# Kernel optimization log

Measured on AMD Instinct MI355X. Metric: run time of the kernel, lower is better.

Reference implementation:

```python
import jax, jax.numpy as jnp
import numpy as np

B, C, N = 2, 1024, 80
D = 3 * C + 2  # 3074 token dim
DFF = 2048     # torch TransformerEncoderLayer default dim_feedforward
HW = 224
REFINE = 3
EPS = 1e-5


def _layernorm(x, g, b):
    m = jnp.mean(x, axis=-1, keepdims=True)
    v = jnp.mean((x - m) ** 2, axis=-1, keepdims=True)
    return g * (x - m) / jnp.sqrt(v + EPS) + b


def _pos_encoding(seq_len, dim):
    pos = jnp.arange(seq_len, dtype=jnp.float32)[:, None]
    div = jnp.exp(jnp.arange(0, dim, 2, dtype=jnp.float32) * (-np.log(10000.0) / dim))
    pe = jnp.zeros((seq_len, dim), dtype=jnp.float32)
    pe = pe.at[:, 0::2].set(jnp.sin(pos * div)).at[:, 1::2].set(jnp.cos(pos * div))
    return pe


def _forward(pre_f, curr_f, first_f, ln_g, ln_b, ipw, ipb, opw, opb,
             n1g, n1b, l1w, l1b, l2w, l2b, n2g, n2b, ow, ob,
             prev_b, first_b):
    # --- vectorized find_best_shift: batched circular L1 correlation ---
    idx = (jnp.arange(N)[None, :] - jnp.arange(N)[:, None]) % N  # [shift, pos]
    rolled = first_b[:, idx]                                     # [B, N, N, 2]
    dist = jnp.abs(prev_b[:, None] - rolled).sum(axis=(-1, -2))  # [B, N]
    best = jnp.argmin(dist, axis=1)                              # first min, like torch loop
    roll_idx = (jnp.arange(N)[None, :] - best[:, None]) % N      # [B, N]
    first_b = jax.vmap(lambda fb, ri: fb[ri])(first_b, roll_idx)

    # --- bilinear upsample to 224x224 (F.interpolate, align_corners=False) ---
    up = lambda f: jax.image.resize(f, (f.shape[0], f.shape[1], HW, HW), method='bilinear')
    pre_up, curr_up, first_up = up(pre_f), up(curr_f), up(first_f)

    # --- vectorized get_bou_features: [B,N,C] gather ---
    gather = jax.vmap(lambda f, b: f[:, b[:, 0], b[:, 1]].T)
    pre_q = gather(pre_up, prev_b)      # [B, N, C]
    first_q = gather(first_up, first_b)  # [B, N, C]

    pe = _pos_encoding(N, D)
    curr = prev_b.astype(jnp.float32)
    scale = 1.0 / jnp.sqrt(jnp.float32(D))
    results = []
    for _ in range(REFINE):
        bf = gather(curr_up, curr.astype(jnp.int32))          # [B, N, C]
        tokens = jnp.concatenate([pre_q, bf, curr, first_q], axis=-1)  # [B, N, D]
        tokens = _layernorm(tokens, ln_g, ln_b)
        tokens = tokens + pe[None]
        # --- TransformerEncoderLayer (post-norm, nhead=1, relu, eval/no dropout) ---
        qkv = tokens @ ipw.T + ipb
        q, k, v = jnp.split(qkv, 3, axis=-1)
        attn = jax.nn.softmax(jnp.einsum('bqd,bkd->bqk', q, k) * scale, axis=-1)
        a = jnp.einsum('bqk,bkd->bqd', attn, v) @ opw.T + opb
        x = _layernorm(tokens + a, n1g, n1b)
        ff = jax.nn.relu(x @ l1w.T + l1b) @ l2w.T + l2b
        x = _layernorm(x + ff, n2g, n2b)
        out = x @ ow.T + ob                                   # [B, N, 1026]
        curr = jnp.clip(curr + out[..., C:], 0.0, 223.0)
        pre_q = pre_q + out[..., :C]
        results.append(curr)
    return jnp.stack(results)  # [REFINE, B, N, 2]


def setup_inputs() -> dict:
    key = jax.random.key(0)
    ks = jax.random.split(key, 12)
    f = lambda i, s: jax.random.normal(ks[i], s, dtype=jnp.float32)
    w = lambda i, s: 0.02 * jax.random.normal(ks[i], s, dtype=jnp.float32)
    return {
        'pre_img_features': f(0, (B, C, 14, 14)),
        'curr_img_features': f(1, (B, C, 14, 14)),
        'first_img_features': f(2, (B, C, 14, 14)),
        'previous_boundary': jax.random.randint(ks[3], (B, N, 2), 0, HW),
        'first_boundary': jax.random.randint(ks[4], (B, N, 2), 0, HW),
        'ln_g': jnp.ones((D,), jnp.float32), 'ln_b': jnp.zeros((D,), jnp.float32),
        'in_proj_w': w(5, (3 * D, D)), 'in_proj_b': jnp.zeros((3 * D,), jnp.float32),
        'out_proj_w': w(6, (D, D)), 'out_proj_b': jnp.zeros((D,), jnp.float32),
        'norm1_g': jnp.ones((D,), jnp.float32), 'norm1_b': jnp.zeros((D,), jnp.float32),
        'lin1_w': w(7, (DFF, D)), 'lin1_b': jnp.zeros((DFF,), jnp.float32),
        'lin2_w': w(8, (D, DFF)), 'lin2_b': jnp.zeros((D,), jnp.float32),
        'norm2_g': jnp.ones((D,), jnp.float32), 'norm2_b': jnp.zeros((D,), jnp.float32),
        'out_w': w(9, (C + 2, D)), 'out_b': jnp.zeros((C + 2,), jnp.float32),
    }


def reference(pre_img_features, curr_img_features, first_img_features,
              previous_boundary, first_boundary,
              ln_g, ln_b, in_proj_w, in_proj_b, out_proj_w, out_proj_b,
              norm1_g, norm1_b, lin1_w, lin1_b, lin2_w, lin2_b,
              norm2_g, norm2_b, out_w, out_b):
    return _forward(pre_img_features, curr_img_features, first_img_features,
                    ln_g, ln_b, in_proj_w, in_proj_b, out_proj_w, out_proj_b,
                    norm1_g, norm1_b, lin1_w, lin1_b, lin2_w, lin2_b,
                    norm2_g, norm2_b, out_w, out_b,
                    previous_boundary, first_boundary)
```

## Files before the change

### kernel.cpp

```cpp
#include <hip/hip_runtime.h>
#include <math.h>

#define B_    2
#define C_    1024
#define N_    80
#define D_    3074
#define DFF_  2048
#define OD_   1026
#define QKV_  9222
#define M_    160
#define EPS_  1e-5f
#define KPD_  3104
#define SPL_  4

typedef __attribute__((ext_vector_type(8))) short bf16x8;
typedef __attribute__((ext_vector_type(4))) float f32x4;

__device__ inline short f2bf(float f) {
    unsigned u = __float_as_uint(f);
    u += 0x7fffu + ((u >> 16) & 1u);
    return (short)(u >> 16);
}

__device__ inline float wave_sum(float v) {
#pragma unroll
    for (int off = 32; off > 0; off >>= 1) v += __shfl_down(v, off, 64);
    return v;
}

__device__ inline float wave_max(float v) {
#pragma unroll
    for (int off = 32; off > 0; off >>= 1) v = fmaxf(v, __shfl_down(v, off, 64));
    return v;
}

__device__ inline void block_reduce_2(float& s, float& s2, float* red) {
    int tid = threadIdx.x;
    int lane = tid & 63, wid = tid >> 6;
    s = wave_sum(s);
    s2 = wave_sum(s2);
    if (lane == 0) { red[wid] = s; red[4 + wid] = s2; }
    __syncthreads();
    if (tid == 0) {
        red[8] = red[0] + red[1] + red[2] + red[3];
        red[9] = red[4] + red[5] + red[6] + red[7];
    }
    __syncthreads();
    s = red[8]; s2 = red[9];
}

__device__ inline void bilin_setup(int p, int& i0, int& i1, float& t) {
    float s = (p + 0.5f) * 0.0625f - 0.5f;
    s = fminf(fmaxf(s, 0.0f), 13.0f);
    i0 = (int)s;
    t = s - (float)i0;
    i1 = min(i0 + 1, 13);
}

__device__ inline float bilin_tap(const float* f, int y0, int y1, float ty,
                                  int x0, int x1, float tx) {
    float a = f[y0 * 14 + x0], b = f[y0 * 14 + x1];
    float c = f[y1 * 14 + x0], d = f[y1 * 14 + x1];
    return (1.f - ty) * ((1.f - tx) * a + tx * b) + ty * ((1.f - tx) * c + tx * d);
}

__global__ __launch_bounds__(128) void align_kernel(const int* __restrict__ prev_b,
                                                    const int* __restrict__ first_b,
                                                    int* __restrict__ fb_al) {
    int b = blockIdx.x;
    int tid = threadIdx.x;
    __shared__ int dist[N_];
    __shared__ int bestIdx;
    if (tid < N_) {
        int s = 0;
        for (int j = 0; j < N_; ++j) {
            int src = (j - tid) % N_;
            if (src < 0) src += N_;
            int dy = prev_b[(b * N_ + j) * 2] - first_b[(b * N_ + src) * 2];
            int dx = prev_b[(b * N_ + j) * 2 + 1] - first_b[(b * N_ + src) * 2 + 1];
            s += abs(dy) + abs(dx);
        }
        dist[tid] = s;
    }
    __syncthreads();
    if (tid == 0) {
        int best = 0, bd = dist[0];
        for (int i = 1; i < N_; ++i)
            if (dist[i] < bd) { bd = dist[i]; best = i; }
        bestIdx = best;
    }
    __syncthreads();
    if (tid < N_) {
        int src = (tid - bestIdx) % N_;
        if (src < 0) src += N_;
        fb_al[(b * N_ + tid) * 2]     = first_b[(b * N_ + src) * 2];
        fb_al[(b * N_ + tid) * 2 + 1] = first_b[(b * N_ + src) * 2 + 1];
    }
}

__global__ __launch_bounds__(256) void gather_init_kernel(
        const float* __restrict__ pre_f, const float* __restrict__ first_f,
        const int* __restrict__ prev_b, const int* __restrict__ fb_al,
        float* __restrict__ pre_q, float* __restrict__ first_q,
        float* __restrict__ curr) {
    int m = blockIdx.x;
    int b = m / N_;
    int tid = threadIdx.x;
    int py = prev_b[m * 2], px = prev_b[m * 2 + 1];
    int fy = fb_al[m * 2], fx = fb_al[m * 2 + 1];
    int py0, py1, px0, px1, fy0, fy1, fx0, fx1;
    float pty, ptx, fty, ftx;
    bilin_setup(py, py0, py1, pty);
    bilin_setup(px, px0, px1, ptx);
    bilin_setup(fy, fy0, fy1, fty);
    bilin_setup(fx, fx0, fx1, ftx);
    for (int c = tid; c < C_; c += 256) {
        const float* fp = pre_f + (size_t)(b * C_ + c) * 196;
        const float* ff = first_f + (size_t)(b * C_ + c) * 196;
        pre_q[(size_t)m * C_ + c]   = bilin_tap(fp, py0, py1, pty, px0, px1, ptx);
        first_q[(size_t)m * C_ + c] = bilin_tap(ff, fy0, fy1, fty, fx0, fx1, ftx);
    }
    if (tid < 2) curr[m * 2 + tid] = (float)prev_b[m * 2 + tid];
}

__global__ __launch_bounds__(256) void pe_kernel(float* __restrict__ pe) {
    int n = blockIdx.x;
    const float negLogDivD = -logf(10000.0f) / (float)D_;
    for (int d = threadIdx.x; d < D_; d += 256) {
        int kk = d >> 1;
        float ang = (float)n * expf((float)(2 * kk) * negLogDivD);
        pe[(size_t)n * D_ + d] = (d & 1) ? cosf(ang) : sinf(ang);
    }
}

__global__ __launch_bounds__(256) void tokens_kernel(
        const float* __restrict__ curr_f, const float* __restrict__ pre_q,
        const float* __restrict__ first_q, const float* __restrict__ curr,
        const float* __restrict__ ln_g, const float* __restrict__ ln_b,
        const float* __restrict__ pe_tab,
        float* __restrict__ tokens, short* __restrict__ tokens_bf) {
    int m = blockIdx.x;
    int b = m / N_;
    int n = m % N_;
    int tid = threadIdx.x;
    __shared__ float bf[C_];
    __shared__ float red[10];

    float cy = curr[m * 2], cx = curr[m * 2 + 1];
    int iy = (int)cy, ix = (int)cx;
    int y0, y1, x0, x1;
    float ty, tx;
    bilin_setup(iy, y0, y1, ty);
    bilin_setup(ix, x0, x1, tx);
    for (int c = tid; c < C_; c += 256) {
        const float* f = curr_f + (size_t)(b * C_ + c) * 196;
        bf[c] = bilin_tap(f, y0, y1, ty, x0, x1, tx);
    }
    __syncthreads();

    float s = 0.f, s2 = 0.f;
    for (int d = tid; d < D_; d += 256) {
        float v;
        if (d < C_)            v = pre_q[(size_t)m * C_ + d];
        else if (d < 2 * C_)   v = bf[d - C_];
        else if (d == 2 * C_)  v = cy;
        else if (d == 2*C_+1)  v = cx;
        else                   v = first_q[(size_t)m * C_ + (d - 2 * C_ - 2)];
        s += v; s2 += v * v;
    }
    block_reduce_2(s, s2, red);
    float mean = s / (float)D_;
    float var = s2 / (float)D_ - mean * mean;
    float inv = rsqrtf(var + EPS_);

    for (int d = tid; d < KPD_; d += 256) {
        if (d < D_) {
            float v;
            if (d < C_)            v = pre_q[(size_t)m * C_ + d];
            else if (d < 2 * C_)   v = bf[d - C_];
            else if (d == 2 * C_)  v = cy;
            else if (d == 2*C_+1)  v = cx;
            else                   v = first_q[(size_t)m * C_ + (d - 2 * C_ - 2)];
            float ln = ln_g[d] * (v - mean) * inv + ln_b[d];
            float val = ln + pe_tab[(size_t)n * D_ + d];
            tokens[(size_t)m * D_ + d] = val;
            tokens_bf[(size_t)m * KPD_ + d] = f2bf(val);
        } else {
            tokens_bf[(size_t)m * KPD_ + d] = 0;
        }
    }
}

#define WPK_CH 25
__global__ __launch_bounds__(256) void wpack_kernel(const float* __restrict__ w,
                                                    short* __restrict__ o,
                                                    int K, int O, int nch) {
    int s = blockIdx.x;
    int nq = (nch + 3) >> 2;
    int c0 = blockIdx.y * nq;
    int c1 = min(nch, c0 + nq);
    int ncq = c1 - c0;
    if (ncq <= 0) return;
    __shared__ short lds[16][WPK_CH * 32 + 8];

    int kbase = c0 * 32;
    int ktot = ncq * 32;
    int npair = ktot >> 1;
    for (int idx = threadIdx.x; idx < 16 * npair; idx += 256) {
        int r = idx / npair;
        int kp = idx % npair;
        int orow = s * 16 + r;
        int k = kbase + kp * 2;
        float2 v = make_float2(0.f, 0.f);
        if (orow < O && k + 1 < K)
            v = *(const float2*)(w + (size_t)orow * K + k);
        lds[r][kp * 2]     = f2bf(v.x);
        lds[r][kp * 2 + 1] = f2bf(v.y);
    }
    __syncthreads();
    for (int idx = threadIdx.x; idx < ncq * 64; idx += 256) {
        int ci = idx >> 6, l = idx & 63;
        int col = l & 15, quad = l >> 4;
        bf16x8 v;
#pragma unroll
        for (int j = 0; j < 8; ++j)
            v[j] = lds[col][ci * 32 + quad * 8 + j];
        *(bf16x8*)(o + ((size_t)s * nch + (c0 + ci)) * 512 + (size_t)l * 8) = v;
    }
}

template <int SW>
__global__ __launch_bounds__(512) void gemm_stage(
        const short* __restrict__ A, const short* __restrict__ Wp,
        const float* __restrict__ bias, float* __restrict__ part,
        int KpA, int nch, int O, int per) {
    int cs = blockIdx.y * per;
    int ce = min(nch, cs + per);
    if (cs >= ce) return;
    int tid = threadIdx.x;
    int lane = tid & 63, wave = tid >> 6;
    int col = lane & 15, quad = lane >> 4;
    int s0 = (blockIdx.x * 8 + wave) * SW;

    __shared__ short lbuf[2][160 * 32];

    int m0 = tid >> 2, p8 = (tid & 3) * 8;
    int m1 = (tid + 512) >> 2;
    const short* a0 = A + (size_t)m0 * KpA + p8;
    const short* a1 = A + (size_t)m1 * KpA + p8;
    bf16x8 sr0, sr1;

    f32x4 acc[SW][10];
#pragma unroll
    for (int j = 0; j < SW; ++j)
#pragma unroll
        for (int t = 0; t < 10; ++t)
#pragma unroll
            for (int r = 0; r < 4; ++r) acc[j][t][r] = 0.f;

    const short* wbase[SW];
#pragma unroll
    for (int j = 0; j < SW; ++j)
        wbase[j] = Wp + (size_t)(s0 + j) * nch * 512 + (size_t)lane * 8;
    bf16x8 wc[SW], wn[SW];

    sr0 = *(const bf16x8*)(a0 + (size_t)cs * 32);
    if (tid < 128) sr1 = *(const bf16x8*)(a1 + (size_t)cs * 32);
#pragma unroll
    for (int j = 0; j < SW; ++j)
        wc[j] = *(const bf16x8*)(wbase[j] + (size_t)cs * 512);
    *(bf16x8*)(&lbuf[0][m0 * 32 + p8]) = sr0;
    if (tid < 128) *(bf16x8*)(&lbuf[0][m1 * 32 + p8]) = sr1;
    __syncthreads();

    int cur = 0;
    for (int c = cs; c < ce; ++c) {
        bool more = (c + 1) < ce;
        if (more) {
            sr0 = *(const bf16x8*)(a0 + (size_t)(c + 1) * 32);
            if (tid < 128) sr1 = *(const bf16x8*)(a1 + (size_t)(c + 1) * 32);
#pragma unroll
            for (int j = 0; j < SW; ++j)
                wn[j] = *(const bf16x8*)(wbase[j] + (size_t)(c + 1) * 512);
        }
#pragma unroll
        for (int t = 0; t < 10; ++t) {
            bf16x8 af = *(const bf16x8*)(&lbuf[cur][t * 512 + col * 32 + quad * 8]);
#pragma unroll
            for (int j = 0; j < SW; ++j)
                acc[j][t] = __builtin_amdgcn_mfma_f32_16x16x32_bf16(af, wc[j], acc[j][t], 0, 0, 0);
        }
        if (more) {
            *(bf16x8*)(&lbuf[cur ^ 1][m0 * 32 + p8]) = sr0;
            if (tid < 128) *(bf16x8*)(&lbuf[cur ^ 1][m1 * 32 + p8]) = sr1;
        }
        __syncthreads();
#pragma unroll
        for (int j = 0; j < SW; ++j) wc[j] = wn[j];
        cur ^= 1;
    }

    float* pout = part + (size_t)blockIdx.y * M_ * O;
#pragma unroll
    for (int j = 0; j < SW; ++j) {
        int oc = (s0 + j) * 16 + col;
        if (oc < O) {
            float bv = (blockIdx.y == 0) ? bias[oc] : 0.f;
#pragma unroll
            for (int t = 0; t < 10; ++t)
#pragma unroll
                for (int r = 0; r < 4; ++r)
                    pout[(size_t)(t * 16 + quad * 4 + r) * O + oc] = acc[j][t][r] + bv;
        }
    }
}

__global__ __launch_bounds__(256) void gemm_mfma_sk(
        const short* __restrict__ A, const float* __restrict__ Wf,
        const float* __restrict__ bias, float* __restrict__ Cout,
        int K, int KpA, int O, int KC) {
    int kc0 = blockIdx.y * KC;
    if (kc0 >= K) return;
    int kend = min(K, kc0 + KC);

    int lane = threadIdx.x & 63;
    int wave = threadIdx.x >> 6;
    int col  = lane & 15;
    int quad = lane >> 4;
    int o0 = blockIdx.x * 128 + wave * 32 + col;
    int o1 = o0 + 16;
    int oc0 = min(o0, O - 1), oc1 = min(o1, O - 1);

    const float* wrow0 = Wf + (size_t)oc0 * K + quad * 8;
    const float* wrow1 = Wf + (size_t)oc1 * K + quad * 8;
    const short* abase = A + (size_t)col * KpA + quad * 8;

    f32x4 acc0[10], acc1[10];
#pragma unroll
    for (int t = 0; t < 10; ++t)
#pragma unroll
        for (int r = 0; r < 4; ++r) { acc0[t][r] = 0.f; acc1[t][r] = 0.f; }

    int nfull = (kend - kc0) >> 5;
    bf16x8 aCur[10];
    float2 wCur[8];
    if (nfull > 0) {
#pragma unroll
        for (int t = 0; t < 10; ++t)
            aCur[t] = *(const bf16x8*)(abase + (size_t)t * 16 * KpA + kc0);
#pragma unroll
        for (int j = 0; j < 4; ++j) {
            wCur[j]     = *(const float2*)(wrow0 + kc0 + 2 * j);
            wCur[4 + j] = *(const float2*)(wrow1 + kc0 + 2 * j);
        }
    }
    for (int i = 0; i < nfull; ++i) {
        bf16x8 aNxt[10];
        float2 wNxt[8];
        if (i + 1 < nfull) {
            int kn = kc0 + (i + 1) * 32;
#pragma unroll
            for (int t = 0; t < 10; ++t)
                aNxt[t] = *(const bf16x8*)(abase + (size_t)t * 16 * KpA + kn);
#pragma unroll
            for (int j = 0; j < 4; ++j) {
                wNxt[j]     = *(const float2*)(wrow0 + kn + 2 * j);
                wNxt[4 + j] = *(const float2*)(wrow1 + kn + 2 * j);
            }
        }
        bf16x8 b0, b1;
#pragma unroll
        for (int j = 0; j < 4; ++j) {
            b0[2*j] = f2bf(wCur[j].x);     b0[2*j+1] = f2bf(wCur[j].y);
            b1[2*j] = f2bf(wCur[4+j].x);   b1[2*j+1] = f2bf(wCur[4+j].y);
        }
#pragma unroll
        for (int t = 0; t < 10; ++t) {
            acc0[t] = __builtin_amdgcn_mfma_f32_16x16x32_bf16(aCur[t], b0, acc0[t], 0, 0, 0);
            acc1[t] = __builtin_amdgcn_mfma_f32_16x16x32_bf16(aCur[t], b1, acc1[t], 0, 0, 0);
        }
#pragma unroll
        for (int t = 0; t < 10; ++t) aCur[t] = aNxt[t];
#pragma unroll
        for (int j = 0; j < 8; ++j) wCur[j] = wNxt[j];
    }
    int kmain = kc0 + nfull * 32;
    if (kmain < kend) {
        bf16x8 b0, b1;
#pragma unroll
        for (int j = 0; j < 8; ++j) {
            int k = kmain + quad * 8 + j;
            b0[j] = (k < kend) ? f2bf(Wf[(size_t)oc0 * K + k]) : (short)0;
            b1[j] = (k < kend) ? f2bf(Wf[(size_t)oc1 * K + k]) : (short)0;
        }
#pragma unroll
        for (int t = 0; t < 10; ++t) {
            bf16x8 af = *(const bf16x8*)(abase + (size_t)t * 16 * KpA + kmain);
            acc0[t] = __builtin_amdgcn_mfma_f32_16x16x32_bf16(af, b0, acc0[t], 0, 0, 0);
            acc1[t] = __builtin_amdgcn_mfma_f32_16x16x32_bf16(af, b1, acc1[t], 0, 0, 0);
        }
    }
    if (o0 < O) {
        float bv = (blockIdx.y == 0) ? bias[o0] : 0.f;
#pragma unroll
        for (int t = 0; t < 10; ++t)
#pragma unroll
            for (int r = 0; r < 4; ++r)
                atomicAdd(&Cout[(size_t)(t * 16 + quad * 4 + r) * O + o0], acc0[t][r] + bv);
    }
    if (o1 < O) {
        float bv = (blockIdx.y == 0) ? bias[o1] : 0.f;
#pragma unroll
        for (int t = 0; t < 10; ++t)
#pragma unroll
            for (int r = 0; r < 4; ++r)
                atomicAdd(&Cout[(size_t)(t * 16 + quad * 4 + r) * O + o1], acc1[t][r] + bv);
    }
}

__global__ __launch_bounds__(256) void relu_cvt_kernel(const float* __restrict__ in,
                                                       int S, size_t sstr,
                                                       short* __restrict__ out,
                                                       int n) {
    int i = blockIdx.x * 256 + threadIdx.x;
    if (i < n) {
        float v = 0.f;
        for (int s = 0; s < S; ++s) v += in[(size_t)s * sstr + i];
        out[i] = f2bf(fmaxf(v, 0.f));
    }
}

__global__ __launch_bounds__(256) void qkv_cvt_kernel(const float* __restrict__ part,
                                                      int S,
                                                      short* __restrict__ q_bf,
                                                      short* __restrict__ k_bf,
                                                      short* __restrict__ v_bf) {
    int m = blockIdx.x;
    int b = m / N_, q = m % N_;
    for (int d = threadIdx.x; d < KPD_; d += 256) {
        short qv = 0, kv = 0, vv = 0;
        if (d < D_) {
            float qf = 0.f, kf = 0.f, vf = 0.f;
            for (int s = 0; s < S; ++s) {
                const float* p = part + (size_t)s * M_ * QKV_ + (size_t)m * QKV_;
                qf += p[d]; kf += p[D_ + d]; vf += p[2 * D_ + d];
            }
            qv = f2bf(qf); kv = f2bf(kf); vv = f2bf(vf);
        }
        q_bf[(size_t)m * KPD_ + d] = qv;
        k_bf[(size_t)m * KPD_ + d] = kv;
        v_bf[((size_t)b * 96 + q) * KPD_ + d] = vv;
    }
}

__global__ __launch_bounds__(256) void scores_mfma(const short* __restrict__ q_bf,
                                                   const short* __restrict__ k_bf,
                                                   float* __restrict__ sc) {
    int bi = blockIdx.x;
    int b = bi / 25, qt = (bi % 25) / 5, kt = bi % 5;
    int lane = threadIdx.x & 63, wave = threadIdx.x >> 6;
    int col = lane & 15, quad = lane >> 4;
    const short* qbase = q_bf + (size_t)(b * N_ + qt * 16 + col) * KPD_ + quad * 8;
    const short* kbase = k_bf + (size_t)(b * N_ + kt * 16 + col) * KPD_ + quad * 8;
    f32x4 acc;
#pragma unroll
    for (int r = 0; r < 4; ++r) acc[r] = 0.f;
    int c0 = wave * 25, c1 = min(97, c0 + 25);
    for (int c = c0; c < c1; ++c) {
        bf16x8 af = *(const bf16x8*)(qbase + c * 32);
        bf16x8 bf8 = *(const bf16x8*)(kbase + c * 32);
        acc = __builtin_amdgcn_mfma_f32_16x16x32_bf16(af, bf8, acc, 0, 0, 0);
    }
    __shared__ f32x4 red[4][64];
    red[wave][lane] = acc;
    __syncthreads();
    if (threadIdx.x < 64) {
        f32x4 t = red[0][lane];
#pragma unroll
        for (int w = 1; w < 4; ++w)
#pragma unroll
            for (int r = 0; r < 4; ++r) t[r] += red[w][lane][r];
        float scale = rsqrtf((float)D_);
#pragma unroll
        for (int r = 0; r < 4; ++r)
            sc[(size_t)(b * N_ + qt * 16 + quad * 4 + r) * N_ + kt * 16 + col] = t[r] * scale;
    }
}

__global__ __launch_bounds__(256) void softmax_kernel(const float* __restrict__ sc,
                                                      short* __restrict__ p_bf) {
    int m = blockIdx.x * 4 + (threadIdx.x >> 6);
    int lane = threadIdx.x & 63;
    const float* row = sc + (size_t)m * N_;
    float a = row[lane];
    float bv = (lane < 16) ? row[64 + lane] : -1e30f;
    float mx = wave_max(fmaxf(a, bv));
    mx = __shfl(mx, 0, 64);
    float e0 = expf(a - mx);
    float e1 = (lane < 16) ? expf(bv - mx) : 0.f;
    float sum = wave_sum(e0 + e1);
    sum = __shfl(sum, 0, 64);
    float rs = 1.0f / sum;
    p_bf[(size_t)m * 96 + lane] = f2bf(e0 * rs);
    if (lane < 32)
        p_bf[(size_t)m * 96 + 64 + lane] = (lane < 16) ? f2bf(e1 * rs) : (short)0;
}

__global__ __launch_bounds__(256) void av_mfma(const short* __restrict__ p_bf,
                                               const short* __restrict__ v_bf,
                                               short* __restrict__ av_bf) {
    int bi = blockIdx.x;
    int b = bi / 49, g = bi % 49;
    int lane = threadIdx.x & 63, wave = threadIdx.x >> 6;
    int dtile = g * 4 + wave;
    if (dtile >= 194) return;
    int d0 = dtile * 16;
    int col = lane & 15, quad = lane >> 4;
    const short* pbase = p_bf + (size_t)b * N_ * 96 + quad * 8;
    const short* vb = v_bf + (size_t)b * 96 * KPD_ + d0 + col;
    f32x4 acc[5];
#pragma unroll
    for (int t = 0; t < 5; ++t)
#pragma unroll
        for (int r = 0; r < 4; ++r) acc[t][r] = 0.f;
#pragma unroll
    for (int c = 0; c < 3; ++c) {
        bf16x8 bf8;
#pragma unroll
        for (int j = 0; j < 8; ++j)
            bf8[j] = vb[(size_t)(c * 32 + quad * 8 + j) * KPD_];
#pragma unroll
        for (int t = 0; t < 5; ++t) {
            bf16x8 af = *(const bf16x8*)(pbase + (size_t)(t * 16 + col) * 96 + c * 32);
            acc[t] = __builtin_amdgcn_mfma_f32_16x16x32_bf16(af, bf8, acc[t], 0, 0, 0);
        }
    }
#pragma unroll
    for (int t = 0; t < 5; ++t)
#pragma unroll
        for (int r = 0; r < 4; ++r)
            av_bf[(size_t)(b * N_ + t * 16 + quad * 4 + r) * KPD_ + d0 + col] = f2bf(acc[t][r]);
}

template <bool WF32>
__global__ __launch_bounds__(256) void ln_kernel(const float* __restrict__ xin,
                                                 int S, size_t sstr,
                                                 const float* __restrict__ res,
                                                 const float* __restrict__ g,
                                                 const float* __restrict__ bta,
                                                 float* __restrict__ outf,
                                                 short* __restrict__ outb) {
    int m = blockIdx.x;
    int tid = threadIdx.x;
    __shared__ float red[10];
    const float* xr = xin + (size_t)m * D_;
    const float* rr = res + (size_t)m * D_;
    float vv[13];
    float s = 0.f, s2 = 0.f;
#pragma unroll
    for (int i = 0; i < 13; ++i) {
        int d = tid + i * 256;
        float v = 0.f;
        if (d < D_) {
            v = rr[d];
            for (int sp = 0; sp < S; ++sp) v += xr[(size_t)sp * sstr + d];
            s += v; s2 += v * v;
        }
        vv[i] = v;
    }
    block_reduce_2(s, s2, red);
    float mean = s / (float)D_;
    float var = s2 / (float)D_ - mean * mean;
    float inv = rsqrtf(var + EPS_);
#pragma unroll
    for (int i = 0; i < 13; ++i) {
        int d = tid + i * 256;
        if (d < D_) {
            float y = g[d] * (vv[i] - mean) * inv + bta[d];
            if (WF32) outf[(size_t)m * D_ + d] = y;
            outb[(size_t)m * KPD_ + d] = f2bf(y);
        } else if (d < KPD_) {
            outb[(size_t)m * KPD_ + d] = 0;
        }
    }
}

__global__ __launch_bounds__(256) void update_kernel(const float* __restrict__ part,
                                                     int S, size_t sstr,
                                                     float* __restrict__ curr,
                                                     float* __restrict__ pre_q,
                                                     float* __restrict__ results) {
    int m = blockIdx.x;
    int tid = threadIdx.x;
    const float* pr = part + (size_t)m * OD_;
    for (int c = tid; c < C_; c += 256) {
        float v = 0.f;
        for (int s = 0; s < S; ++s) v += pr[(size_t)s * sstr + c];
        pre_q[(size_t)m * C_ + c] += v;
    }
    if (tid < 2) {
        float v = 0.f;
        for (int s = 0; s < S; ++s) v += pr[(size_t)s * sstr + C_ + tid];
        float nc = curr[m * 2 + tid] + v;
        nc = fminf(fmaxf(nc, 0.f), 223.f);
        curr[m * 2 + tid] = nc;
        results[m * 2 + tid] = nc;
    }
}

extern "C" void kernel_launch(void* const* d_in, const int* in_sizes, int n_in,
                              void* d_out, int out_size, void* d_ws, size_t ws_size,
                              hipStream_t stream) {
    const float* pre_f   = (const float*)d_in[0];
    const float* curr_f  = (const float*)d_in[1];
    const float* first_f = (const float*)d_in[2];
    const int*   prev_b  = (const int*)d_in[3];
    const int*   first_b = (const int*)d_in[4];
    const float* ln_g    = (const float*)d_in[5];
    const float* ln_b    = (const float*)d_in[6];
    const float* ipw     = (const float*)d_in[7];
    const float* ipb     = (const float*)d_in[8];
    const float* opw     = (const float*)d_in[9];
    const float* opb     = (const float*)d_in[10];
    const float* n1g     = (const float*)d_in[11];
    const float* n1b     = (const float*)d_in[12];
    const float* l1w     = (const float*)d_in[13];
    const float* l1b     = (const float*)d_in[14];
    const float* l2w     = (const float*)d_in[15];
    const float* l2b     = (const float*)d_in[16];
    const float* n2g     = (const float*)d_in[17];
    const float* n2b     = (const float*)d_in[18];
    const float* ow      = (const float*)d_in[19];
    const float* ob      = (const float*)d_in[20];
    float* outp = (float*)d_out;

    float* wf = (float*)d_ws;
    size_t off = 0;
    int*   fb_al   = (int*)(wf + off); off += 320;
    float* curr    = wf + off;         off += 320;
    float* pre_q   = wf + off;         off += (size_t)M_ * C_;
    float* first_q = wf + off;         off += (size_t)M_ * C_;
    float* tokens  = wf + off;         off += (size_t)M_ * D_;
    float* xbuf    = wf + off;         off += (size_t)M_ * D_;
    float* sc      = wf + off;         off += (size_t)M_ * N_;
    float* pe_tab  = wf + off;         off += (size_t)N_ * D_;
    short* tokens_bf = (short*)(wf + off); off += (size_t)M_ * KPD_ / 2;
    short* x_bf      = (short*)(wf + off); off += (size_t)M_ * KPD_ / 2;
    short* x2_bf     = (short*)(wf + off); off += (size_t)M_ * KPD_ / 2;
    short* av_bf     = (short*)(wf + off); off += (size_t)M_ * KPD_ / 2;
    short* ff1_bf    = (short*)(wf + off); off += (size_t)M_ * DFF_ / 2;
    short* q_bf      = (short*)(wf + off); off += (size_t)M_ * KPD_ / 2;
    short* k_bf      = (short*)(wf + off); off += (size_t)M_ * KPD_ / 2;
    short* v_bf      = (short*)(wf + off); off += (size_t)B_ * 96 * KPD_ / 2;
    short* p_bf      = (short*)(wf + off); off += (size_t)M_ * 96 / 2;
    size_t commonF = off;

    size_t o2 = commonF;
    short* ipw_p2 = (short*)(wf + o2); o2 += (size_t)592 * 97 * 256;
    short* opw_p2 = (short*)(wf + o2); o2 += (size_t)208 * 97 * 256;
    short* l1w_p2 = (short*)(wf + o2); o2 += (size_t)128 * 97 * 256;
    short* l2w_p2 = (short*)(wf + o2); o2 += (size_t)208 * 64 * 256;
    short* ow_p2  = (short*)(wf + o2); o2 += (size_t)80  * 97 * 256;
    float* gpart  = wf + o2;           o2 += (size_t)SPL_ * M_ * QKV_;

    size_t o0 = commonF;
    float* qkv   = wf + o0; o0 += (size_t)M_ * QKV_;
    float* aout  = wf + o0; o0 += (size_t)M_ * D_;
    float* ff1f  = wf + o0; o0 += (size_t)M_ * DFF_;
    float* ffout = wf + o0; o0 += (size_t)M_ * D_;
    float* outb  = wf + o0; o0 += (size_t)M_ * OD_;

    int tier = (ws_size >= o2 * sizeof(float)) ? 2 : 0;
    (void)in_sizes; (void)n_in; (void)out_size;

    hipLaunchKernelGGL(align_kernel, dim3(B_), dim3(128), 0, stream,
                       prev_b, first_b, fb_al);
    hipLaunchKernelGGL(gather_init_kernel, dim3(M_), dim3(256), 0, stream,
                       pre_f, first_f, prev_b, fb_al, pre_q, first_q, curr);
    hipLaunchKernelGGL(pe_kernel, dim3(N_), dim3(256), 0, stream, pe_tab);
    hipMemsetAsync(v_bf, 0, (size_t)B_ * 96 * KPD_ * 2, stream);

    if (tier == 2) {
        hipLaunchKernelGGL(wpack_kernel, dim3(592, 4), dim3(256), 0, stream, ipw, ipw_p2, D_, QKV_, 97);
        hipLaunchKernelGGL(wpack_kernel, dim3(208, 4), dim3(256), 0, stream, opw, opw_p2, D_, D_, 97);
        hipLaunchKernelGGL(wpack_kernel, dim3(128, 4), dim3(256), 0, stream, l1w, l1w_p2, D_, DFF_, 97);
        hipLaunchKernelGGL(wpack_kernel, dim3(208, 4), dim3(256), 0, stream, l2w, l2w_p2, DFF_, D_, 64);
        hipLaunchKernelGGL(wpack_kernel, dim3(80, 4),  dim3(256), 0, stream, ow, ow_p2, D_, OD_, 97);
    }

    for (int it = 0; it < 3; ++it) {
        if (tier == 0) {
            hipMemsetAsync(qkv,   0, (size_t)M_ * QKV_ * 4, stream);
            hipMemsetAsync(aout,  0, (size_t)M_ * D_   * 4, stream);
            hipMemsetAsync(ff1f,  0, (size_t)M_ * DFF_ * 4, stream);
            hipMemsetAsync(ffout, 0, (size_t)M_ * D_   * 4, stream);
            hipMemsetAsync(outb,  0, (size_t)M_ * OD_  * 4, stream);
        }

        hipLaunchKernelGGL(tokens_kernel, dim3(M_), dim3(256), 0, stream,
                           curr_f, pre_q, first_q, curr, ln_g, ln_b, pe_tab,
                           tokens, tokens_bf);
        if (tier == 2)
            hipLaunchKernelGGL((gemm_stage<2>), dim3(37, SPL_), dim3(512), 0, stream,
                               tokens_bf, ipw_p2, ipb, gpart, KPD_, 97, QKV_, 25);
        else
            hipLaunchKernelGGL(gemm_mfma_sk, dim3(73, 6), dim3(256), 0, stream,
                               tokens_bf, ipw, ipb, qkv, D_, KPD_, QKV_, 544);
        hipLaunchKernelGGL(qkv_cvt_kernel, dim3(M_), dim3(256), 0, stream,
                           (tier == 2) ? gpart : qkv, (tier == 2) ? SPL_ : 1,
                           q_bf, k_bf, v_bf);
        hipLaunchKernelGGL(scores_mfma, dim3(50), dim3(256), 0, stream,
                           q_bf, k_bf, sc);
        hipLaunchKernelGGL(softmax_kernel, dim3(40), dim3(256), 0, stream,
                           sc, p_bf);
        hipLaunchKernelGGL(av_mfma, dim3(98), dim3(256), 0, stream,
                           p_bf, v_bf, av_bf);
        if (tier == 2)
            hipLaunchKernelGGL((gemm_stage<2>), dim3(13, SPL_), dim3(512), 0, stream,
                               av_bf, opw_p2, opb, gpart, KPD_, 97, D_, 25);
        else
            hipLaunchKernelGGL(gemm_mfma_sk, dim3(25, 10), dim3(256), 0, stream,
                               av_bf, opw, opb, aout, D_, KPD_, D_, 320);
        hipLaunchKernelGGL((ln_kernel<true>), dim3(M_), dim3(256), 0, stream,
                           (tier == 2) ? gpart : aout, (tier == 2) ? SPL_ : 1, (size_t)M_ * D_,
                           tokens, n1g, n1b, xbuf, x_bf);
        if (tier == 2)
            hipLaunchKernelGGL((gemm_stage<2>), dim3(8, SPL_), dim3(512), 0, stream,
                               x_bf, l1w_p2, l1b, gpart, KPD_, 97, DFF_, 25);
        else
            hipLaunchKernelGGL(gemm_mfma_sk, dim3(16, 17), dim3(256), 0, stream,
                               x_bf, l1w, l1b, ff1f, D_, KPD_, DFF_, 192);
        hipLaunchKernelGGL(relu_cvt_kernel, dim3((M_ * DFF_ + 255) / 256), dim3(256), 0, stream,
                           (tier == 2) ? gpart : ff1f, (tier == 2) ? SPL_ : 1, (size_t)M_ * DFF_,
                           ff1_bf, M_ * DFF_);
        if (tier == 2)
            hipLaunchKernelGGL((gemm_stage<2>), dim3(13, SPL_), dim3(512), 0, stream,
                               ff1_bf, l2w_p2, l2b, gpart, DFF_, 64, D_, 16);
        else
            hipLaunchKernelGGL(gemm_mfma_sk, dim3(25, 11), dim3(256), 0, stream,
                               ff1_bf, l2w, l2b, ffout, DFF_, DFF_, D_, 192);
        hipLaunchKernelGGL((ln_kernel<false>), dim3(M_), dim3(256), 0, stream,
                           (tier == 2) ? gpart : ffout, (tier == 2) ? SPL_ : 1, (size_t)M_ * D_,
                           xbuf, n2g, n2b, (float*)nullptr, x2_bf);
        if (tier == 2)
            hipLaunchKernelGGL((gemm_stage<2>), dim3(5, SPL_), dim3(512), 0, stream,
                               x2_bf, ow_p2, ob, gpart, KPD_, 97, OD_, 25);
        else
            hipLaunchKernelGGL(gemm_mfma_sk, dim3(9, 13), dim3(256), 0, stream,
                               x2_bf, ow, ob, outb, D_, KPD_, OD_, 256);
        hipLaunchKernelGGL(update_kernel, dim3(M_), dim3(256), 0, stream,
                           (tier == 2) ? gpart : outb, (tier == 2) ? SPL_ : 1, (size_t)M_ * OD_,
                           curr, pre_q, outp + (size_t)it * M_ * 2);
    }
}
```

Before: 1.090 ms.

## Retune split-K per GEMM, fuse scores with softmax, faster weight packing

```diff
diff --git a/kernel.cpp b/kernel.cpp
--- a/kernel.cpp
+++ b/kernel.cpp
@@ -11,7 +11,17 @@
 #define M_    160
 #define EPS_  1e-5f
 #define KPD_  3104
-#define SPL_  4
+
+#define SQKV 4
+#define PQKV 25
+#define SOP  8
+#define POP  13
+#define SFF1 11
+#define PFF1 9
+#define SFF2 8
+#define PFF2 8
+#define SHD  11
+#define PHD  9
 
 typedef __attribute__((ext_vector_type(8))) short bf16x8;
 typedef __attribute__((ext_vector_type(4))) float f32x4;
@@ -22,15 +32,13 @@
     return (short)(u >> 16);
 }
 
+__device__ inline int pack2bf(float lo, float hi) {
+    return (int)(unsigned short)f2bf(lo) | ((int)(unsigned short)f2bf(hi) << 16);
+}
+
 __device__ inline float wave_sum(float v) {
 #pragma unroll
     for (int off = 32; off > 0; off >>= 1) v += __shfl_down(v, off, 64);
-    return v;
-}
-
-__device__ inline float wave_max(float v) {
-#pragma unroll
-    for (int off = 32; off > 0; off >>= 1) v = fmaxf(v, __shfl_down(v, off, 64));
     return v;
 }
 
@@ -191,42 +199,42 @@
     }
 }
 
-#define WPK_CH 25
-__global__ __launch_bounds__(256) void wpack_kernel(const float* __restrict__ w,
-                                                    short* __restrict__ o,
-                                                    int K, int O, int nch) {
-    int s = blockIdx.x;
-    int nq = (nch + 3) >> 2;
-    int c0 = blockIdx.y * nq;
-    int c1 = min(nch, c0 + nq);
-    int ncq = c1 - c0;
-    if (ncq <= 0) return;
-    __shared__ short lds[16][WPK_CH * 32 + 8];
-
-    int kbase = c0 * 32;
-    int ktot = ncq * 32;
-    int npair = ktot >> 1;
-    for (int idx = threadIdx.x; idx < 16 * npair; idx += 256) {
-        int r = idx / npair;
-        int kp = idx % npair;
-        int orow = s * 16 + r;
-        int k = kbase + kp * 2;
-        float2 v = make_float2(0.f, 0.f);
-        if (orow < O && k + 1 < K)
-            v = *(const float2*)(w + (size_t)orow * K + k);
-        lds[r][kp * 2]     = f2bf(v.x);
-        lds[r][kp * 2 + 1] = f2bf(v.y);
-    }
-    __syncthreads();
-    for (int idx = threadIdx.x; idx < ncq * 64; idx += 256) {
-        int ci = idx >> 6, l = idx & 63;
-        int col = l & 15, quad = l >> 4;
-        bf16x8 v;
-#pragma unroll
-        for (int j = 0; j < 8; ++j)
-            v[j] = lds[col][ci * 32 + quad * 8 + j];
-        *(bf16x8*)(o + ((size_t)s * nch + (c0 + ci)) * 512 + (size_t)l * 8) = v;
-    }
+__global__ __launch_bounds__(256) void wpack2(const float* __restrict__ w,
+                                              short* __restrict__ o,
+                                              int K, int O, int nch, int ntiles) {
+    int gw = (int)((blockIdx.x * 256 + threadIdx.x) >> 6);
+    if (gw >= ntiles) return;
+    int lane = threadIdx.x & 63;
+    int strip = gw / nch, chunk = gw - strip * nch;
+    int row = strip * 16 + (lane >> 2);
+    int k0 = chunk * 32 + (lane & 3) * 8;
+    float f[8];
+    if (row < O && k0 + 8 <= K) {
+        const float* src = w + (size_t)row * K + k0;
+        float2 a = *(const float2*)(src);
+        float2 b = *(const float2*)(src + 2);
+        float2 c = *(const float2*)(src + 4);
+        float2 d = *(const float2*)(src + 6);
+        f[0]=a.x; f[1]=a.y; f[2]=b.x; f[3]=b.y;
+        f[4]=c.x; f[5]=c.y; f[6]=d.x; f[7]=d.y;
+    } else {
+#pragma unroll
+        for (int j = 0; j < 8; ++j) {
+            int k = k0 + j;
+            f[j] = (row < O && k < K) ? w[(size_t)row * K + k] : 0.f;
+        }
+    }
+    int p0 = pack2bf(f[0], f[1]);
+    int p1 = pack2bf(f[2], f[3]);
+    int p2 = pack2bf(f[4], f[5]);
+    int p3 = pack2bf(f[6], f[7]);
+    int src = (lane & 15) * 4 + (lane >> 4);
+    int4 out;
+    out.x = __shfl(p0, src, 64);
+    out.y = __shfl(p1, src, 64);
+    out.z = __shfl(p2, src, 64);
+    out.w = __shfl(p3, src, 64);
+    *(int4*)(o + (size_t)gw * 512 + (size_t)lane * 8) = out;
 }
 
 template <int SW>
@@ -435,8 +443,14 @@
                                                       short* __restrict__ q_bf,
                                                       short* __restrict__ k_bf,
                                                       short* __restrict__ v_bf) {
-    int m = blockIdx.x;
-    int b = m / N_, q = m % N_;
+    int mb = blockIdx.x;
+    int b = mb / 96, q = mb % 96;
+    if (q >= N_) {
+        for (int d = threadIdx.x; d < KPD_; d += 256)
+            v_bf[((size_t)b * 96 + q) * KPD_ + d] = 0;
+        return;
+    }
+    int m = b * N_ + q;
     for (int d = threadIdx.x; d < KPD_; d += 256) {
         short qv = 0, kv = 0, vv = 0;
         if (d < D_) {
@@ -453,57 +467,71 @@
     }
 }
 
-__global__ __launch_bounds__(256) void scores_mfma(const short* __restrict__ q_bf,
-                                                   const short* __restrict__ k_bf,
-                                                   float* __restrict__ sc) {
+__global__ __launch_bounds__(256) void attn_sc(const short* __restrict__ q_bf,
+                                               const short* __restrict__ k_bf,
+                                               short* __restrict__ p_bf) {
     int bi = blockIdx.x;
-    int b = bi / 25, qt = (bi % 25) / 5, kt = bi % 5;
+    int b = bi / 5, qt = bi % 5;
     int lane = threadIdx.x & 63, wave = threadIdx.x >> 6;
     int col = lane & 15, quad = lane >> 4;
     const short* qbase = q_bf + (size_t)(b * N_ + qt * 16 + col) * KPD_ + quad * 8;
-    const short* kbase = k_bf + (size_t)(b * N_ + kt * 16 + col) * KPD_ + quad * 8;
-    f32x4 acc;
-#pragma unroll
-    for (int r = 0; r < 4; ++r) acc[r] = 0.f;
+    const short* kb = k_bf + (size_t)(b * N_ + col) * KPD_ + quad * 8;
+
+    f32x4 acc[5];
+#pragma unroll
+    for (int kt = 0; kt < 5; ++kt)
+#pragma unroll
+        for (int r = 0; r < 4; ++r) acc[kt][r] = 0.f;
+
     int c0 = wave * 25, c1 = min(97, c0 + 25);
     for (int c = c0; c < c1; ++c) {
-        bf16x8 af = *(const bf16x8*)(qbase + c * 32);
-        bf16x8 bf8 = *(const bf16x8*)(kbase + c * 32);
-        acc = __builtin_amdgcn_mfma_f32_16x16x32_bf16(af, bf8, acc, 0, 0, 0);
-    }
-    __shared__ f32x4 red[4][64];
-    red[wave][lane] = acc;
+        bf16x8 af = *(const bf16x8*)(qbase + (size_t)c * 32);
+#pragma unroll
+        for (int kt = 0; kt < 5; ++kt) {
+            bf16x8 kf = *(const bf16x8*)(kb + (size_t)(kt * 16) * KPD_ + (size_t)c * 32);
+            acc[kt] = __builtin_amdgcn_mfma_f32_16x16x32_bf16(af, kf, acc[kt], 0, 0, 0);
+        }
+    }
+
+    __shared__ f32x4 red[4][5][64];
+    __shared__ float sl[16][80];
+#pragma unroll
+    for (int kt = 0; kt < 5; ++kt) red[wave][kt][lane] = acc[kt];
     __syncthreads();
-    if (threadIdx.x < 64) {
-        f32x4 t = red[0][lane];
+    float scale = rsqrtf((float)D_);
+    for (int item = threadIdx.x; item < 320; item += 256) {
+        int kt = item >> 6, l2 = item & 63;
+        int c2 = l2 & 15, q2 = l2 >> 4;
+        f32x4 v = red[0][kt][l2];
 #pragma unroll
         for (int w = 1; w < 4; ++w)
 #pragma unroll
-            for (int r = 0; r < 4; ++r) t[r] += red[w][lane][r];
-        float scale = rsqrtf((float)D_);
+            for (int r = 0; r < 4; ++r) v[r] += red[w][kt][l2][r];
 #pragma unroll
         for (int r = 0; r < 4; ++r)
-            sc[(size_t)(b * N_ + qt * 16 + quad * 4 + r) * N_ + kt * 16 + col] = t[r] * scale;
-    }
-}
-
-__global__ __launch_bounds__(256) void softmax_kernel(const float* __restrict__ sc,
-                                                      short* __restrict__ p_bf) {
-    int m = blockIdx.x * 4 + (threadIdx.x >> 6);
-    int lane = threadIdx.x & 63;
-    const float* row = sc + (size_t)m * N_;
-    float a = row[lane];
-    float bv = (lane < 16) ? row[64 + lane] : -1e30f;
-    float mx = wave_max(fmaxf(a, bv));
-    mx = __shfl(mx, 0, 64);
-    float e0 = expf(a - mx);
-    float e1 = (lane < 16) ? expf(bv - mx) : 0.f;
-    float sum = wave_sum(e0 + e1);
-    sum = __shfl(sum, 0, 64);
+            sl[q2 * 4 + r][kt * 16 + c2] = v[r] * scale;
+    }
+    __syncthreads();
+
+    int r = wave * 4 + (lane >> 4);
+    int cb = lane & 15;
+    float v[5];
+    float mx = -1e30f;
+#pragma unroll
+    for (int i = 0; i < 5; ++i) { v[i] = sl[r][cb + 16 * i]; mx = fmaxf(mx, v[i]); }
+#pragma unroll
+    for (int off = 1; off < 16; off <<= 1) mx = fmaxf(mx, __shfl_xor(mx, off, 64));
+    float e[5];
+    float sum = 0.f;
+#pragma unroll
+    for (int i = 0; i < 5; ++i) { e[i] = expf(v[i] - mx); sum += e[i]; }
+#pragma unroll
+    for (int off = 1; off < 16; off <<= 1) sum += __shfl_xor(sum, off, 64);
     float rs = 1.0f / sum;
-    p_bf[(size_t)m * 96 + lane] = f2bf(e0 * rs);
-    if (lane < 32)
-        p_bf[(size_t)m * 96 + 64 + lane] = (lane < 16) ? f2bf(e1 * rs) : (short)0;
+    size_t m96 = (size_t)(b * N_ + qt * 16 + r) * 96;
+#pragma unroll
+    for (int i = 0; i < 5; ++i) p_bf[m96 + cb + 16 * i] = f2bf(e[i] * rs);
+    p_bf[m96 + 80 + cb] = 0;
 }
 
 __global__ __launch_bounds__(256) void av_mfma(const short* __restrict__ p_bf,
@@ -642,7 +670,6 @@
     float* first_q = wf + off;         off += (size_t)M_ * C_;
     float* tokens  = wf + off;         off += (size_t)M_ * D_;
     float* xbuf    = wf + off;         off += (size_t)M_ * D_;
-    float* sc      = wf + off;         off += (size_t)M_ * N_;
     float* pe_tab  = wf + off;         off += (size_t)N_ * D_;
     short* tokens_bf = (short*)(wf + off); off += (size_t)M_ * KPD_ / 2;
     short* x_bf      = (short*)(wf + off); off += (size_t)M_ * KPD_ / 2;
@@ -661,7 +688,7 @@
     short* l1w_p2 = (short*)(wf + o2); o2 += (size_t)128 * 97 * 256;
     short* l2w_p2 = (short*)(wf + o2); o2 += (size_t)208 * 64 * 256;
     short* ow_p2  = (short*)(wf + o2); o2 += (size_t)80  * 97 * 256;
-    float* gpart  = wf + o2;           o2 += (size_t)SPL_ * M_ * QKV_;
+    float* gpart  = wf + o2;           o2 += (size_t)SQKV * M_ * QKV_;
 
     size_t o0 = commonF;
     float* qkv   = wf + o0; o0 += (size_t)M_ * QKV_;
@@ -678,14 +705,18 @@
     hipLaunchKernelGGL(gather_init_kernel, dim3(M_), dim3(256), 0, stream,
                        pre_f, first_f, prev_b, fb_al, pre_q, first_q, curr);
     hipLaunchKernelGGL(pe_kernel, dim3(N_), dim3(256), 0, stream, pe_tab);
-    hipMemsetAsync(v_bf, 0, (size_t)B_ * 96 * KPD_ * 2, stream);
 
     if (tier == 2) {
-        hipLaunchKernelGGL(wpack_kernel, dim3(592, 4), dim3(256), 0, stream, ipw, ipw_p2, D_, QKV_, 97);
-        hipLaunchKernelGGL(wpack_kernel, dim3(208, 4), dim3(256), 0, stream, opw, opw_p2, D_, D_, 97);
-        hipLaunchKernelGGL(wpack_kernel, dim3(128, 4), dim3(256), 0, stream, l1w, l1w_p2, D_, DFF_, 97);
-        hipLaunchKernelGGL(wpack_kernel, dim3(208, 4), dim3(256), 0, stream, l2w, l2w_p2, DFF_, D_, 64);
-        hipLaunchKernelGGL(wpack_kernel, dim3(80, 4),  dim3(256), 0, stream, ow, ow_p2, D_, OD_, 97);
+        hipLaunchKernelGGL(wpack2, dim3(592 * 97 / 4), dim3(256), 0, stream,
+                           ipw, ipw_p2, D_, QKV_, 97, 592 * 97);
+        hipLaunchKernelGGL(wpack2, dim3(208 * 97 / 4), dim3(256), 0, stream,
+                           opw, opw_p2, D_, D_, 97, 208 * 97);
+        hipLaunchKernelGGL(wpack2, dim3(128 * 97 / 4), dim3(256), 0, stream,
+                           l1w, l1w_p2, D_, DFF_, 97, 128 * 97);
+        hipLaunchKernelGGL(wpack2, dim3(208 * 64 / 4), dim3(256), 0, stream,
+                           l2w, l2w_p2, DFF_, D_, 64, 208 * 64);
+        hipLaunchKernelGGL(wpack2, dim3(80 * 97 / 4), dim3(256), 0, stream,
+                           ow, ow_p2, D_, OD_, 97, 80 * 97);
     }
 
     for (int it = 0; it < 3; ++it) {
@@ -701,55 +732,53 @@
                            curr_f, pre_q, first_q, curr, ln_g, ln_b, pe_tab,
                            tokens, tokens_bf);
         if (tier == 2)
-            hipLaunchKernelGGL((gemm_stage<2>), dim3(37, SPL_), dim3(512), 0, stream,
-                               tokens_bf, ipw_p2, ipb, gpart, KPD_, 97, QKV_, 25);
+            hipLaunchKernelGGL((gemm_stage<2>), dim3(37, SQKV), dim3(512), 0, stream,
+                               tokens_bf, ipw_p2, ipb, gpart, KPD_, 97, QKV_, PQKV);
         else
             hipLaunchKernelGGL(gemm_mfma_sk, dim3(73, 6), dim3(256), 0, stream,
                                tokens_bf, ipw, ipb, qkv, D_, KPD_, QKV_, 544);
-        hipLaunchKernelGGL(qkv_cvt_kernel, dim3(M_), dim3(256), 0, stream,
-                           (tier == 2) ? gpart : qkv, (tier == 2) ? SPL_ : 1,
+        hipLaunchKernelGGL(qkv_cvt_kernel, dim3(B_ * 96), dim3(256), 0, stream,
+                           (tier == 2) ? gpart : qkv, (tier == 2) ? SQKV : 1,
                            q_bf, k_bf, v_bf);
-        hipLaunchKernelGGL(scores_mfma, dim3(50), dim3(256), 0, stream,
-                           q_bf, k_bf, sc);
-        hipLaunchKernelGGL(softmax_kernel, dim3(40), dim3(256), 0, stream,
-                           sc, p_bf);
+        hipLaunchKernelGGL(attn_sc, dim3(B_ * 5), dim3(256), 0, stream,
+                           q_bf, k_bf, p_bf);
         hipLaunchKernelGGL(av_mfma, dim3(98), dim3(256), 0, stream,
                            p_bf, v_bf, av_bf);
         if (tier == 2)
-            hipLaunchKernelGGL((gemm_stage<2>), dim3(13, SPL_), dim3(512), 0, stream,
-                               av_bf, opw_p2, opb, gpart, KPD_, 97, D_, 25);
+            hipLaunchKernelGGL((gemm_stage<2>), dim3(13, SOP), dim3(512), 0, stream,
+                               av_bf, opw_p2, opb, gpart, KPD_, 97, D_, POP);
         else
             hipLaunchKernelGGL(gemm_mfma_sk, dim3(25, 10), dim3(256), 0, stream,
                                av_bf, opw, opb, aout, D_, KPD_, D_, 320);
         hipLaunchKernelGGL((ln_kernel<true>), dim3(M_), dim3(256), 0, stream,
-                           (tier == 2) ? gpart : aout, (tier == 2) ? SPL_ : 1, (size_t)M_ * D_,
+                           (tier == 2) ? gpart : aout, (tier == 2) ? SOP : 1, (size_t)M_ * D_,
                            tokens, n1g, n1b, xbuf, x_bf);
         if (tier == 2)
-            hipLaunchKernelGGL((gemm_stage<2>), dim3(8, SPL_), dim3(512), 0, stream,
-                               x_bf, l1w_p2, l1b, gpart, KPD_, 97, DFF_, 25);
+            hipLaunchKernelGGL((gemm_stage<2>), dim3(8, SFF1), dim3(512), 0, stream,
+                               x_bf, l1w_p2, l1b, gpart, KPD_, 97, DFF_, PFF1);
         else
             hipLaunchKernelGGL(gemm_mfma_sk, dim3(16, 17), dim3(256), 0, stream,
                                x_bf, l1w, l1b, ff1f, D_, KPD_, DFF_, 192);
         hipLaunchKernelGGL(relu_cvt_kernel, dim3((M_ * DFF_ + 255) / 256), dim3(256), 0, stream,
-                           (tier == 2) ? gpart : ff1f, (tier == 2) ? SPL_ : 1, (size_t)M_ * DFF_,
+                           (tier == 2) ? gpart : ff1f, (tier == 2) ? SFF1 : 1, (size_t)M_ * DFF_,
                            ff1_bf, M_ * DFF_);
         if (tier == 2)
-            hipLaunchKernelGGL((gemm_stage<2>), dim3(13, SPL_), dim3(512), 0, stream,
-                               ff1_bf, l2w_p2, l2b, gpart, DFF_, 64, D_, 16);
+            hipLaunchKernelGGL((gemm_stage<2>), dim3(13, SFF2), dim3(512), 0, stream,
+                               ff1_bf, l2w_p2, l2b, gpart, DFF_, 64, D_, PFF2);
         else
             hipLaunchKernelGGL(gemm_mfma_sk, dim3(25, 11), dim3(256), 0, stream,
                                ff1_bf, l2w, l2b, ffout, DFF_, DFF_, D_, 192);
         hipLaunchKernelGGL((ln_kernel<false>), dim3(M_), dim3(256), 0, stream,
-                           (tier == 2) ? gpart : ffout, (tier == 2) ? SPL_ : 1, (size_t)M_ * D_,
+                           (tier == 2) ? gpart : ffout, (tier == 2) ? SFF2 : 1, (size_t)M_ * D_,
                            xbuf, n2g, n2b, (float*)nullptr, x2_bf);
         if (tier == 2)
-            hipLaunchKernelGGL((gemm_stage<2>), dim3(5, SPL_), dim3(512), 0, stream,
-                               x2_bf, ow_p2, ob, gpart, KPD_, 97, OD_, 25);
+            hipLaunchKernelGGL((gemm_stage<2>), dim3(5, SHD), dim3(512), 0, stream,
+                               x2_bf, ow_p2, ob, gpart, KPD_, 97, OD_, PHD);
         else
             hipLaunchKernelGGL(gemm_mfma_sk, dim3(9, 13), dim3(256), 0, stream,
                                x2_bf, ow, ob, outb, D_, KPD_, OD_, 256);
         hipLaunchKernelGGL(update_kernel, dim3(M_), dim3(256), 0, stream,
-                           (tier == 2) ? gpart : outb, (tier == 2) ? SPL_ : 1, (size_t)M_ * OD_,
+                           (tier == 2) ? gpart : outb, (tier == 2) ? SHD : 1, (size_t)M_ * OD_,
                            curr, pre_q, outp + (size_t)it * M_ * 2);
     }
 }
```

Result: faster. 1.022 ms (-6.3%).
